# Optimization experiments

Hardware: AMD Instinct MI355X
Metric: run time of the kernel (lower is better)

## Reference

```python
import jax, jax.numpy as jnp
import numpy as np

N_NODES = 100000
N_EDGES = 3200000
D_IN, D_HID, D_OUT = 128, 64, 64


def setup_inputs() -> dict:
    key = jax.random.key(0)
    ks = jax.random.split(key, 8)
    x = jax.random.normal(ks[0], (N_NODES, D_IN), dtype=jnp.float32)
    edge_index = jax.random.randint(ks[1], (2, N_EDGES), 0, N_NODES, dtype=jnp.int32)
    # Glorot-ish init for GCN weights, zero bias (PyG default)
    def w(k, fi, fo):
        s = (6.0 / (fi + fo)) ** 0.5
        return jax.random.uniform(k, (fi, fo), jnp.float32, -s, s)
    return {
        "x": x,
        "edge_index": edge_index,
        "W1": w(ks[2], D_IN, D_HID), "b1": jnp.zeros((D_HID,), jnp.float32),
        "W2": w(ks[3], D_HID, D_HID), "b2": jnp.zeros((D_HID,), jnp.float32),
        "W3": w(ks[4], D_HID, D_OUT), "b3": jnp.zeros((D_OUT,), jnp.float32),
    }


def _gcn_layer(x, W, b, src, dst, norm, num_nodes):
    # GCNConv: out[i] = sum_{j->i} norm_ji * (x W)[j] + b   (self-loops included in src/dst)
    h = x @ W                                   # [N, F_out] small GEMM
    msg = h[src] * norm[:, None]                # [E+N, F_out] gather
    out = jax.ops.segment_sum(msg, dst, num_segments=num_nodes)  # scatter-add
    return out + b


def reference(x, edge_index, W1, b1, W2, b2, W3, b3):
    n = x.shape[0]
    loop = jnp.arange(n, dtype=edge_index.dtype)
    src = jnp.concatenate([edge_index[0], loop])  # add self-loops (GCN default)
    dst = jnp.concatenate([edge_index[1], loop])
    # symmetric normalization: deg^{-1/2}[src] * deg^{-1/2}[dst]
    deg = jax.ops.segment_sum(jnp.ones_like(dst, dtype=x.dtype), dst, num_segments=n)
    dinv = jnp.where(deg > 0, jax.lax.rsqrt(deg), 0.0)
    norm = dinv[src] * dinv[dst]

    h = jax.nn.relu(_gcn_layer(x, W1, b1, src, dst, norm, n))
    h = jax.nn.relu(_gcn_layer(h, W2, b2, src, dst, norm, n))
    out = _gcn_layer(h, W3, b3, src, dst, norm, n)
    return out
```

## Files before the change

### kernel.cpp

```cpp
#include <hip/hip_runtime.h>
#include <hip/hip_bf16.h>

static inline size_t align256(size_t x) { return (x + 255) & ~(size_t)255; }

#define BSTRIDE 9216

typedef float vf2 __attribute__((ext_vector_type(2)));


__global__ void cursor_init_kernel(int* __restrict__ cursor, int nb) {
    int b = blockIdx.x * blockDim.x + threadIdx.x;
    if (b < nb) cursor[b] = b * BSTRIDE;
}

__global__ __launch_bounds__(1024) void partition_place_kernel(const int* __restrict__ src,
                                                               const int* __restrict__ dst,
                                                               int* __restrict__ cursor,
                                                               unsigned int* __restrict__ part,
                                                               int e, int nb, int tile) {
    __shared__ int hist[512];
    __shared__ int base[512];
    const int t = threadIdx.x;
    const int lo = blockIdx.x * tile;
    const int hi = min(lo + tile, e);
    for (int i = t; i < nb; i += 1024) hist[i] = 0;
    __syncthreads();
    for (int i = lo + t; i < hi; i += 1024) atomicAdd(&hist[dst[i] >> 8], 1);
    __syncthreads();
    for (int i = t; i < nb; i += 1024) {
        int c = hist[i];
        base[i] = c ? atomicAdd(&cursor[i], c) : 0;
        hist[i] = 0;
    }
    __syncthreads();
    for (int i = lo + t; i < hi; i += 1024) {
        int s = src[i], d = dst[i];
        int b = d >> 8;
        int p = base[b] + atomicAdd(&hist[b], 1);
        part[p] = ((unsigned int)s << 8) | (unsigned int)(d & 255);
    }
}

__global__ __launch_bounds__(512) void cursor_scan_kernel(const int* __restrict__ cursor,
                                                          int* __restrict__ bstart, int nb) {
    __shared__ int lds[512];
    const int t = threadIdx.x;
    int v = (t < nb) ? (cursor[t] - t * BSTRIDE) : 0;
    lds[t] = v;
    __syncthreads();
    for (int off = 1; off < 512; off <<= 1) {
        int add = (t >= off) ? lds[t - off] : 0;
        __syncthreads();
        lds[t] += add;
        __syncthreads();
    }
    if (t < nb) {
        bstart[t] = lds[t] - v;
        if (t == nb - 1) bstart[nb] = lds[t];
    }
}

__global__ __launch_bounds__(1024) void csr_build_place_kernel(const unsigned int* __restrict__ part,
                                                               const int* __restrict__ bstart,
                                                               int* __restrict__ row_ptr,
                                                               float* __restrict__ dinv,
                                                               int* __restrict__ col, int n) {
    __shared__ int cnt[256];
    __shared__ int scan[256];
    __shared__ int cur[256];
    const int t = threadIdx.x;
    const int node0 = blockIdx.x << 8;
    const int o0 = bstart[blockIdx.x];
    const int m = bstart[blockIdx.x + 1] - o0;
    const int p0 = blockIdx.x * BSTRIDE;
    if (t < 256) cnt[t] = 0;
    __syncthreads();
    for (int i = t; i < m; i += 1024) atomicAdd(&cnt[part[p0 + i] & 255u], 1);
    __syncthreads();
    const int v = (t < 256) ? cnt[t] : 0;
    if (t < 256) scan[t] = v;
    __syncthreads();
    for (int off = 1; off < 256; off <<= 1) {
        int add = (t >= off && t < 256) ? scan[t - off] : 0;
        __syncthreads();
        if (t < 256) scan[t] += add;
        __syncthreads();
    }
    if (t < 256) {
        const int node = node0 + t;
        const int excl = o0 + scan[t] - v;
        cur[t] = excl;
        if (node < n) {
            row_ptr[node] = excl;
            dinv[node] = rsqrtf((float)(v + 1));
            if (node == n - 1) row_ptr[n] = o0 + m;
        }
    }
    __syncthreads();
    for (int i = t; i < m; i += 1024) {
        unsigned int sd = part[p0 + i];
        int p = atomicAdd(&cur[sd & 255u], 1);
        col[p] = (int)(sd >> 8);
    }
}


__device__ __forceinline__ unsigned int bf16rne(float f) {
    unsigned int u = __float_as_uint(f);
    return (u + 0x7fffu + ((u >> 16) & 1u)) >> 16;
}
__device__ __forceinline__ unsigned int bf16pack(float a, float b) {
    return bf16rne(a) | (bf16rne(b) << 16);
}

__device__ __forceinline__ vf2 bf2f(unsigned int u) {
    float2 f = __bfloat1622float2(*(const __hip_bfloat162*)&u);
    vf2 r; r.x = f.x; r.y = f.y;
    return r;
}
__device__ __forceinline__ void bf8add(vf2* a, uint4 v) {
    a[0] += bf2f(v.x);
    a[1] += bf2f(v.y);
    a[2] += bf2f(v.z);
    a[3] += bf2f(v.w);
}


template<int K>
__global__ __launch_bounds__(256) void gemm_scale(const float* __restrict__ A,
                                                  const float* __restrict__ W,
                                                  const float* __restrict__ dinv,
                                                  unsigned int* __restrict__ gout, int n) {
    constexpr int KC = 64;
    constexpr int ROWS = 128;
    constexpr int LDX = KC + 4;
    __shared__ float xs[ROWS * LDX];
    __shared__ float ws[KC * 64];
    const int t = threadIdx.x;
    const int r0 = blockIdx.x * ROWS;
    const int rt = t >> 3;
    const int c4 = (t & 7) * 2;

    float acc[4][8];
#pragma unroll
    for (int a = 0; a < 4; ++a)
#pragma unroll
        for (int b = 0; b < 8; ++b) acc[a][b] = 0.f;

    for (int kc = 0; kc < K; kc += KC) {
        {
            const float4* Wg = (const float4*)(W + kc * 64);
            for (int i = t; i < KC * 16; i += 256) ((float4*)ws)[i] = Wg[i];
        }
        {
            const int jr = t >> 4;
            const int j = t & 15;
            for (int r = jr; r < ROWS; r += 16) {
                const int gr = r0 + r;
                float4 v = make_float4(0.f, 0.f, 0.f, 0.f);
                if (gr < n) v = ((const float4*)A)[(size_t)gr * (K / 4) + (kc >> 2) + j];
                *(float4*)&xs[r * LDX + j * 4] = v;
            }
        }
        __syncthreads();
#pragma unroll 4
        for (int k = 0; k < KC; ++k) {
            const float4 w0 = ((const float4*)ws)[k * 16 + c4];
            const float4 w1 = ((const float4*)ws)[k * 16 + c4 + 1];
#pragma unroll
            for (int rr = 0; rr < 4; ++rr) {
                const float xv = xs[(rt + rr * 32) * LDX + k];
                acc[rr][0] = fmaf(xv, w0.x, acc[rr][0]);
                acc[rr][1] = fmaf(xv, w0.y, acc[rr][1]);
                acc[rr][2] = fmaf(xv, w0.z, acc[rr][2]);
                acc[rr][3] = fmaf(xv, w0.w, acc[rr][3]);
                acc[rr][4] = fmaf(xv, w1.x, acc[rr][4]);
                acc[rr][5] = fmaf(xv, w1.y, acc[rr][5]);
                acc[rr][6] = fmaf(xv, w1.z, acc[rr][6]);
                acc[rr][7] = fmaf(xv, w1.w, acc[rr][7]);
            }
        }
        __syncthreads();
    }
#pragma unroll
    for (int rr = 0; rr < 4; ++rr) {
        const int gr = r0 + rt + rr * 32;
        if (gr < n) {
            const float d = dinv[gr];
            uint4 o;
            o.x = bf16pack(acc[rr][0] * d, acc[rr][1] * d);
            o.y = bf16pack(acc[rr][2] * d, acc[rr][3] * d);
            o.z = bf16pack(acc[rr][4] * d, acc[rr][5] * d);
            o.w = bf16pack(acc[rr][6] * d, acc[rr][7] * d);
            ((uint4*)gout)[(size_t)gr * 8 + (t & 7)] = o;
        }
    }
}


__device__ __forceinline__ void gather_agg8(const uint4* __restrict__ g,
                                            const int* __restrict__ row_ptr,
                                            const int* __restrict__ col,
                                            int node, int fc, vf2* acc) {
    bf8add(acc, g[(size_t)node * 8 + fc]);
    int e = row_ptr[node];
    const int e1 = row_ptr[node + 1];
    while (e < e1 && (e & 3)) { bf8add(acc, g[(size_t)col[e] * 8 + fc]); ++e; }
    for (; e + 8 <= e1; e += 8) {
        const int4 c0 = *(const int4*)(col + e);
        const int4 c1 = *(const int4*)(col + e + 4);
        uint4 v0 = g[(size_t)c0.x * 8 + fc];
        uint4 v1 = g[(size_t)c0.y * 8 + fc];
        uint4 v2 = g[(size_t)c0.z * 8 + fc];
        uint4 v3 = g[(size_t)c0.w * 8 + fc];
        uint4 v4 = g[(size_t)c1.x * 8 + fc];
        uint4 v5 = g[(size_t)c1.y * 8 + fc];
        uint4 v6 = g[(size_t)c1.z * 8 + fc];
        uint4 v7 = g[(size_t)c1.w * 8 + fc];
        bf8add(acc, v0); bf8add(acc, v1); bf8add(acc, v2); bf8add(acc, v3);
        bf8add(acc, v4); bf8add(acc, v5); bf8add(acc, v6); bf8add(acc, v7);
    }
    if (e + 4 <= e1) {
        const int4 c0 = *(const int4*)(col + e);
        uint4 v0 = g[(size_t)c0.x * 8 + fc];
        uint4 v1 = g[(size_t)c0.y * 8 + fc];
        uint4 v2 = g[(size_t)c0.z * 8 + fc];
        uint4 v3 = g[(size_t)c0.w * 8 + fc];
        bf8add(acc, v0); bf8add(acc, v1); bf8add(acc, v2); bf8add(acc, v3);
        e += 4;
    }
    for (; e < e1; ++e) bf8add(acc, g[(size_t)col[e] * 8 + fc]);
}


__global__ __launch_bounds__(256) void fused_agg_gemm_kernel(const uint4* __restrict__ g,
                                                             const int* __restrict__ row_ptr,
                                                             const int* __restrict__ col,
                                                             const float* __restrict__ dinv,
                                                             const float* __restrict__ bias,
                                                             const float* __restrict__ W,
                                                             unsigned int* __restrict__ gout,
                                                             int n) {
    __shared__ float ws[64 * 64];
    __shared__ float hs[32 * 68];
    const int t = threadIdx.x;
    const int r = t >> 3;
    const int fc = t & 7;
    const int node = blockIdx.x * 32 + r;
    const bool valid = node < n;

    for (int i = t; i < 1024; i += 256) ((float4*)ws)[i] = ((const float4*)W)[i];

    vf2 acc[4];
    acc[0] = vf2{0.f, 0.f}; acc[1] = vf2{0.f, 0.f};
    acc[2] = vf2{0.f, 0.f}; acc[3] = vf2{0.f, 0.f};
    if (valid) {
        gather_agg8(g, row_ptr, col, node, fc, acc);
        const float d = dinv[node];
        const float4 b0 = ((const float4*)bias)[fc * 2];
        const float4 b1 = ((const float4*)bias)[fc * 2 + 1];
        acc[0].x = fmaxf(fmaf(acc[0].x, d, b0.x), 0.f);
        acc[0].y = fmaxf(fmaf(acc[0].y, d, b0.y), 0.f);
        acc[1].x = fmaxf(fmaf(acc[1].x, d, b0.z), 0.f);
        acc[1].y = fmaxf(fmaf(acc[1].y, d, b0.w), 0.f);
        acc[2].x = fmaxf(fmaf(acc[2].x, d, b1.x), 0.f);
        acc[2].y = fmaxf(fmaf(acc[2].y, d, b1.y), 0.f);
        acc[3].x = fmaxf(fmaf(acc[3].x, d, b1.z), 0.f);
        acc[3].y = fmaxf(fmaf(acc[3].y, d, b1.w), 0.f);
    }
    *(float4*)&hs[r * 68 + fc * 8]     = make_float4(acc[0].x, acc[0].y, acc[1].x, acc[1].y);
    *(float4*)&hs[r * 68 + fc * 8 + 4] = make_float4(acc[2].x, acc[2].y, acc[3].x, acc[3].y);
    __syncthreads();

    float a0 = 0.f, a1 = 0.f, a2 = 0.f, a3 = 0.f;
    float a4 = 0.f, a5 = 0.f, a6 = 0.f, a7 = 0.f;
#pragma unroll 8
    for (int k = 0; k < 64; ++k) {
        const float hv = hs[r * 68 + k];
        const float4 w0 = ((const float4*)ws)[k * 16 + fc * 2];
        const float4 w1 = ((const float4*)ws)[k * 16 + fc * 2 + 1];
        a0 = fmaf(hv, w0.x, a0);
        a1 = fmaf(hv, w0.y, a1);
        a2 = fmaf(hv, w0.z, a2);
        a3 = fmaf(hv, w0.w, a3);
        a4 = fmaf(hv, w1.x, a4);
        a5 = fmaf(hv, w1.y, a5);
        a6 = fmaf(hv, w1.z, a6);
        a7 = fmaf(hv, w1.w, a7);
    }
    if (valid) {
        const float d2 = dinv[node];
        uint4 o;
        o.x = bf16pack(a0 * d2, a1 * d2);
        o.y = bf16pack(a2 * d2, a3 * d2);
        o.z = bf16pack(a4 * d2, a5 * d2);
        o.w = bf16pack(a6 * d2, a7 * d2);
        ((uint4*)gout)[(size_t)node * 8 + fc] = o;
    }
}


__global__ __launch_bounds__(256) void aggregate_kernel(const uint4* __restrict__ g,
                                                        const int* __restrict__ row_ptr,
                                                        const int* __restrict__ col,
                                                        const float* __restrict__ dinv,
                                                        const float* __restrict__ bias,
                                                        float4* __restrict__ out,
                                                        int n) {
    const int t = threadIdx.x;
    const int node = blockIdx.x * 32 + (t >> 3);
    const int fc = t & 7;
    if (node >= n) return;
    vf2 acc[4];
    acc[0] = vf2{0.f, 0.f}; acc[1] = vf2{0.f, 0.f};
    acc[2] = vf2{0.f, 0.f}; acc[3] = vf2{0.f, 0.f};
    gather_agg8(g, row_ptr, col, node, fc, acc);
    const float d = dinv[node];
    const float4 b0 = ((const float4*)bias)[fc * 2];
    const float4 b1 = ((const float4*)bias)[fc * 2 + 1];
    float4 o0, o1;
    o0.x = fmaf(acc[0].x, d, b0.x);
    o0.y = fmaf(acc[0].y, d, b0.y);
    o0.z = fmaf(acc[1].x, d, b0.z);
    o0.w = fmaf(acc[1].y, d, b0.w);
    o1.x = fmaf(acc[2].x, d, b1.x);
    o1.y = fmaf(acc[2].y, d, b1.y);
    o1.z = fmaf(acc[3].x, d, b1.z);
    o1.w = fmaf(acc[3].y, d, b1.w);
    out[(size_t)node * 16 + fc * 2]     = o0;
    out[(size_t)node * 16 + fc * 2 + 1] = o1;
}


extern "C" void kernel_launch(void* const* d_in, const int* in_sizes, int n_in,
                              void* d_out, int out_size, void* d_ws, size_t ws_size,
                              hipStream_t stream) {
    const float* x  = (const float*)d_in[0];
    const int*   ei = (const int*)d_in[1];
    const float* W1 = (const float*)d_in[2];
    const float* b1 = (const float*)d_in[3];
    const float* W2 = (const float*)d_in[4];
    const float* b2 = (const float*)d_in[5];
    const float* W3 = (const float*)d_in[6];
    const float* b3 = (const float*)d_in[7];
    float* out = (float*)d_out;

    const int n = in_sizes[0] / 128;
    const int e = in_sizes[1] / 2;
    const int* srcv = ei;
    const int* dstv = ei + e;

    char* ws = (char*)d_ws;
    size_t off = 0;
    float* dinv   = (float*)(ws + off); off = align256(off + (size_t)n * 4);
    int* row_ptr  = (int*)(ws + off);   off = align256(off + (size_t)(n + 1) * 4);
    int* bstart   = (int*)(ws + off);   off = align256(off + 1024 * 4);
    int* cursor   = (int*)(ws + off);   off = align256(off + 1024 * 4);
    int* col      = (int*)(ws + off);   off = align256(off + (size_t)e * 4);
    unsigned int* gbuf  = (unsigned int*)(ws + off); off = align256(off + (size_t)n * 64 * 2);
    unsigned int* gbuf2 = (unsigned int*)(ws + off); off = align256(off + (size_t)n * 64 * 2);
    unsigned int* part  = gbuf;
    (void)ws_size; (void)n_in; (void)out_size;

    const int nbkt = (n + 255) >> 8;

    cursor_init_kernel<<<2, 512, 0, stream>>>(cursor, nbkt);
    const int G = 400;
    const int tile = (e + G - 1) / G;
    partition_place_kernel<<<G, 1024, 0, stream>>>(srcv, dstv, cursor, part, e, nbkt, tile);
    cursor_scan_kernel<<<1, 512, 0, stream>>>(cursor, bstart, nbkt);
    csr_build_place_kernel<<<nbkt, 1024, 0, stream>>>(part, bstart, row_ptr, dinv, col, n);

    const int gemm_grid = (n + 127) / 128;
    const int agg_grid = (n + 31) / 32;

    gemm_scale<128><<<gemm_grid, 256, 0, stream>>>(x, W1, dinv, gbuf, n);
    fused_agg_gemm_kernel<<<agg_grid, 256, 0, stream>>>((const uint4*)gbuf, row_ptr, col,
                                                        dinv, b1, W2, gbuf2, n);
    fused_agg_gemm_kernel<<<agg_grid, 256, 0, stream>>>((const uint4*)gbuf2, row_ptr, col,
                                                        dinv, b2, W3, gbuf, n);
    aggregate_kernel<<<agg_grid, 256, 0, stream>>>((const uint4*)gbuf, row_ptr, col,
                                                   dinv, b3, (float4*)out, n);
}
```

Baseline: 392.4 us.

## Make aggregation kernels persistent with atomic chunk counters

The fused aggregate+GEMM and final aggregate kernels now run a fixed grid of persistent blocks. Each block repeatedly grabs 32-node chunks from a global atomic counter; the three counters are zeroed in the cursor init kernel. This loads the weight matrix into LDS once per persistent block rather than once per 32-node chunk, and balances irregular degree distributions dynamically. In exchange it adds an atomic plus two barriers per chunk, and drops the barrier between writing and reading the per-row LDS tile, which relies on each row being handled within a single wavefront.

```diff
diff --git a/kernel.cpp b/kernel.cpp
--- a/kernel.cpp
+++ b/kernel.cpp
@@ -11,6 +11,7 @@
 __global__ void cursor_init_kernel(int* __restrict__ cursor, int nb) {
     int b = blockIdx.x * blockDim.x + threadIdx.x;
     if (b < nb) cursor[b] = b * BSTRIDE;
+    if (b >= 512 && b < 515) cursor[b] = 0;
 }
 
 __global__ __launch_bounds__(1024) void partition_place_kernel(const int* __restrict__ src,
@@ -240,62 +241,72 @@
                                                              const float* __restrict__ bias,
                                                              const float* __restrict__ W,
                                                              unsigned int* __restrict__ gout,
-                                                             int n) {
+                                                             int* __restrict__ ctr,
+                                                             int nch, int n) {
     __shared__ float ws[64 * 64];
     __shared__ float hs[32 * 68];
+    __shared__ int s_c;
     const int t = threadIdx.x;
     const int r = t >> 3;
     const int fc = t & 7;
-    const int node = blockIdx.x * 32 + r;
-    const bool valid = node < n;
 
     for (int i = t; i < 1024; i += 256) ((float4*)ws)[i] = ((const float4*)W)[i];
 
-    vf2 acc[4];
-    acc[0] = vf2{0.f, 0.f}; acc[1] = vf2{0.f, 0.f};
-    acc[2] = vf2{0.f, 0.f}; acc[3] = vf2{0.f, 0.f};
-    if (valid) {
-        gather_agg8(g, row_ptr, col, node, fc, acc);
-        const float d = dinv[node];
-        const float4 b0 = ((const float4*)bias)[fc * 2];
-        const float4 b1 = ((const float4*)bias)[fc * 2 + 1];
-        acc[0].x = fmaxf(fmaf(acc[0].x, d, b0.x), 0.f);
-        acc[0].y = fmaxf(fmaf(acc[0].y, d, b0.y), 0.f);
-        acc[1].x = fmaxf(fmaf(acc[1].x, d, b0.z), 0.f);
-        acc[1].y = fmaxf(fmaf(acc[1].y, d, b0.w), 0.f);
-        acc[2].x = fmaxf(fmaf(acc[2].x, d, b1.x), 0.f);
-        acc[2].y = fmaxf(fmaf(acc[2].y, d, b1.y), 0.f);
-        acc[3].x = fmaxf(fmaf(acc[3].x, d, b1.z), 0.f);
-        acc[3].y = fmaxf(fmaf(acc[3].y, d, b1.w), 0.f);
-    }
-    *(float4*)&hs[r * 68 + fc * 8]     = make_float4(acc[0].x, acc[0].y, acc[1].x, acc[1].y);
-    *(float4*)&hs[r * 68 + fc * 8 + 4] = make_float4(acc[2].x, acc[2].y, acc[3].x, acc[3].y);
-    __syncthreads();
-
-    float a0 = 0.f, a1 = 0.f, a2 = 0.f, a3 = 0.f;
-    float a4 = 0.f, a5 = 0.f, a6 = 0.f, a7 = 0.f;
+    for (;;) {
+        __syncthreads();
+        if (t == 0) s_c = atomicAdd(ctr, 1);
+        __syncthreads();
+        const int c = s_c;
+        if (c >= nch) break;
+
+        const int node = c * 32 + r;
+        const bool valid = node < n;
+
+        vf2 acc[4];
+        acc[0] = vf2{0.f, 0.f}; acc[1] = vf2{0.f, 0.f};
+        acc[2] = vf2{0.f, 0.f}; acc[3] = vf2{0.f, 0.f};
+        if (valid) {
+            gather_agg8(g, row_ptr, col, node, fc, acc);
+            const float d = dinv[node];
+            const float4 b0 = ((const float4*)bias)[fc * 2];
+            const float4 b1 = ((const float4*)bias)[fc * 2 + 1];
+            acc[0].x = fmaxf(fmaf(acc[0].x, d, b0.x), 0.f);
+            acc[0].y = fmaxf(fmaf(acc[0].y, d, b0.y), 0.f);
+            acc[1].x = fmaxf(fmaf(acc[1].x, d, b0.z), 0.f);
+            acc[1].y = fmaxf(fmaf(acc[1].y, d, b0.w), 0.f);
+            acc[2].x = fmaxf(fmaf(acc[2].x, d, b1.x), 0.f);
+            acc[2].y = fmaxf(fmaf(acc[2].y, d, b1.y), 0.f);
+            acc[3].x = fmaxf(fmaf(acc[3].x, d, b1.z), 0.f);
+            acc[3].y = fmaxf(fmaf(acc[3].y, d, b1.w), 0.f);
+        }
+        *(float4*)&hs[r * 68 + fc * 8]     = make_float4(acc[0].x, acc[0].y, acc[1].x, acc[1].y);
+        *(float4*)&hs[r * 68 + fc * 8 + 4] = make_float4(acc[2].x, acc[2].y, acc[3].x, acc[3].y);
+
+        float a0 = 0.f, a1 = 0.f, a2 = 0.f, a3 = 0.f;
+        float a4 = 0.f, a5 = 0.f, a6 = 0.f, a7 = 0.f;
 #pragma unroll 8
-    for (int k = 0; k < 64; ++k) {
-        const float hv = hs[r * 68 + k];
-        const float4 w0 = ((const float4*)ws)[k * 16 + fc * 2];
-        const float4 w1 = ((const float4*)ws)[k * 16 + fc * 2 + 1];
-        a0 = fmaf(hv, w0.x, a0);
-        a1 = fmaf(hv, w0.y, a1);
-        a2 = fmaf(hv, w0.z, a2);
-        a3 = fmaf(hv, w0.w, a3);
-        a4 = fmaf(hv, w1.x, a4);
-        a5 = fmaf(hv, w1.y, a5);
-        a6 = fmaf(hv, w1.z, a6);
-        a7 = fmaf(hv, w1.w, a7);
-    }
-    if (valid) {
-        const float d2 = dinv[node];
-        uint4 o;
-        o.x = bf16pack(a0 * d2, a1 * d2);
-        o.y = bf16pack(a2 * d2, a3 * d2);
-        o.z = bf16pack(a4 * d2, a5 * d2);
-        o.w = bf16pack(a6 * d2, a7 * d2);
-        ((uint4*)gout)[(size_t)node * 8 + fc] = o;
+        for (int k = 0; k < 64; ++k) {
+            const float hv = hs[r * 68 + k];
+            const float4 w0 = ((const float4*)ws)[k * 16 + fc * 2];
+            const float4 w1 = ((const float4*)ws)[k * 16 + fc * 2 + 1];
+            a0 = fmaf(hv, w0.x, a0);
+            a1 = fmaf(hv, w0.y, a1);
+            a2 = fmaf(hv, w0.z, a2);
+            a3 = fmaf(hv, w0.w, a3);
+            a4 = fmaf(hv, w1.x, a4);
+            a5 = fmaf(hv, w1.y, a5);
+            a6 = fmaf(hv, w1.z, a6);
+            a7 = fmaf(hv, w1.w, a7);
+        }
+        if (valid) {
+            const float d2 = dinv[node];
+            uint4 o;
+            o.x = bf16pack(a0 * d2, a1 * d2);
+            o.y = bf16pack(a2 * d2, a3 * d2);
+            o.z = bf16pack(a4 * d2, a5 * d2);
+            o.w = bf16pack(a6 * d2, a7 * d2);
+            ((uint4*)gout)[(size_t)node * 8 + fc] = o;
+        }
     }
 }
 
@@ -306,29 +317,38 @@
                                                         const float* __restrict__ dinv,
                                                         const float* __restrict__ bias,
                                                         float4* __restrict__ out,
-                                                        int n) {
-    const int t = threadIdx.x;
-    const int node = blockIdx.x * 32 + (t >> 3);
+                                                        int* __restrict__ ctr,
+                                                        int nch, int n) {
+    __shared__ int s_c;
+    const int t = threadIdx.x;
     const int fc = t & 7;
-    if (node >= n) return;
-    vf2 acc[4];
-    acc[0] = vf2{0.f, 0.f}; acc[1] = vf2{0.f, 0.f};
-    acc[2] = vf2{0.f, 0.f}; acc[3] = vf2{0.f, 0.f};
-    gather_agg8(g, row_ptr, col, node, fc, acc);
-    const float d = dinv[node];
-    const float4 b0 = ((const float4*)bias)[fc * 2];
-    const float4 b1 = ((const float4*)bias)[fc * 2 + 1];
-    float4 o0, o1;
-    o0.x = fmaf(acc[0].x, d, b0.x);
-    o0.y = fmaf(acc[0].y, d, b0.y);
-    o0.z = fmaf(acc[1].x, d, b0.z);
-    o0.w = fmaf(acc[1].y, d, b0.w);
-    o1.x = fmaf(acc[2].x, d, b1.x);
-    o1.y = fmaf(acc[2].y, d, b1.y);
-    o1.z = fmaf(acc[3].x, d, b1.z);
-    o1.w = fmaf(acc[3].y, d, b1.w);
-    out[(size_t)node * 16 + fc * 2]     = o0;
-    out[(size_t)node * 16 + fc * 2 + 1] = o1;
+    for (;;) {
+        __syncthreads();
+        if (t == 0) s_c = atomicAdd(ctr, 1);
+        __syncthreads();
+        const int c = s_c;
+        if (c >= nch) break;
+        const int node = c * 32 + (t >> 3);
+        if (node >= n) continue;
+        vf2 acc[4];
+        acc[0] = vf2{0.f, 0.f}; acc[1] = vf2{0.f, 0.f};
+        acc[2] = vf2{0.f, 0.f}; acc[3] = vf2{0.f, 0.f};
+        gather_agg8(g, row_ptr, col, node, fc, acc);
+        const float d = dinv[node];
+        const float4 b0 = ((const float4*)bias)[fc * 2];
+        const float4 b1 = ((const float4*)bias)[fc * 2 + 1];
+        float4 o0, o1;
+        o0.x = fmaf(acc[0].x, d, b0.x);
+        o0.y = fmaf(acc[0].y, d, b0.y);
+        o0.z = fmaf(acc[1].x, d, b0.z);
+        o0.w = fmaf(acc[1].y, d, b0.w);
+        o1.x = fmaf(acc[2].x, d, b1.x);
+        o1.y = fmaf(acc[2].y, d, b1.y);
+        o1.z = fmaf(acc[3].x, d, b1.z);
+        o1.w = fmaf(acc[3].y, d, b1.w);
+        out[(size_t)node * 16 + fc * 2]     = o0;
+        out[(size_t)node * 16 + fc * 2 + 1] = o1;
+    }
 }
 
 
@@ -372,13 +392,18 @@
     csr_build_place_kernel<<<nbkt, 1024, 0, stream>>>(part, bstart, row_ptr, dinv, col, n);
 
     const int gemm_grid = (n + 127) / 128;
-    const int agg_grid = (n + 31) / 32;
+    const int nch = (n + 31) / 32;
+    const int fused_grid = 1536;
+    const int agg_grid = 2048;
 
     gemm_scale<128><<<gemm_grid, 256, 0, stream>>>(x, W1, dinv, gbuf, n);
-    fused_agg_gemm_kernel<<<agg_grid, 256, 0, stream>>>((const uint4*)gbuf, row_ptr, col,
-                                                        dinv, b1, W2, gbuf2, n);
-    fused_agg_gemm_kernel<<<agg_grid, 256, 0, stream>>>((const uint4*)gbuf2, row_ptr, col,
-                                                        dinv, b2, W3, gbuf, n);
+    fused_agg_gemm_kernel<<<fused_grid, 256, 0, stream>>>((const uint4*)gbuf, row_ptr, col,
+                                                          dinv, b1, W2, gbuf2,
+                                                          &cursor[512], nch, n);
+    fused_agg_gemm_kernel<<<fused_grid, 256, 0, stream>>>((const uint4*)gbuf2, row_ptr, col,
+                                                          dinv, b2, W3, gbuf,
+                                                          &cursor[513], nch, n);
     aggregate_kernel<<<agg_grid, 256, 0, stream>>>((const uint4*)gbuf, row_ptr, col,
-                                                   dinv, b3, (float4*)out, n);
-}
+                                                   dinv, b3, (float4*)out,
+                                                   &cursor[514], nch, n);
+}
```

After: 475.4 us. +21.1%, slower.
